# Performance work log

Hardware: AMD Instinct MI355X
Metric: run time of the kernel (lower is better)

The kernel has to match this reference:

```python
import jax, jax.numpy as jnp
import numpy as np

NUM_HEADS = 8
CODEBOOK_SIZE = 1024
HEAD_DIM = 128
BATCH = 32768


def setup_inputs() -> dict:
    key = jax.random.key(0)
    k_z, k_cb = jax.random.split(key)
    z = jax.random.normal(k_z, (BATCH, NUM_HEADS * HEAD_DIM), dtype=jnp.float32)
    codebooks = jax.random.normal(k_cb, (NUM_HEADS, CODEBOOK_SIZE, HEAD_DIM), dtype=jnp.float32)
    return {"z": z, "codebooks": codebooks}


def reference(z, codebooks):
    # z: [B, H*D]; codebooks: [H, K, D]
    H, K, D = codebooks.shape
    B = z.shape[0]
    zh = z.reshape(B, H, D)
    # Squared euclidean distances ||z - c||^2 = ||z||^2 - 2 z.c + ||c||^2.
    # torch.cdist(p=2) applies sqrt, but sqrt is monotone so argmin is identical.
    z_sq = jnp.sum(zh * zh, axis=-1)                       # [B, H]
    c_sq = jnp.sum(codebooks * codebooks, axis=-1)         # [H, K]
    cross = jnp.einsum('bhd,hkd->bhk', zh, codebooks)      # [B, H, K]
    d2 = z_sq[:, :, None] - 2.0 * cross + c_sq[None, :, :]  # [B, H, K]
    idx = jnp.argmin(d2, axis=-1)                          # [B, H] int
    # Gather nearest codes per head: codebooks[h, idx[b,h]] -> [B, H, D]
    zq = codebooks[jnp.arange(H)[None, :], idx]
    # Straight-through estimator: forward = codes, backward = identity on z.
    zq = zh + jax.lax.stop_gradient(zq - zh)
    return zq.reshape(B, H * D), idx
```

## Files before the change

kernel.cpp:

```cpp
#include <hip/hip_runtime.h>

namespace {
constexpr int kNH = 8;
constexpr int kK  = 1024;
constexpr int kD  = 128;
constexpr int kB  = 32768;

constexpr int BM  = 128;
constexpr int kMarginQ = 4;
constexpr float kMarginF32 = 0.0625f;

constexpr size_t kOffCsq  = 4096;
constexpr size_t kOffCbF  = 65536;
constexpr size_t kOffPart = 65536 + 4194304;
constexpr size_t kOffWl6  = 65536 + 8388608;
constexpr size_t kOffWl5  = 65536 + 4194304;
}

typedef short           bf16x8 __attribute__((ext_vector_type(8)));
typedef unsigned short  us16x8 __attribute__((ext_vector_type(8)));
typedef float           f32x16 __attribute__((ext_vector_type(16)));

__device__ __forceinline__ unsigned short f2bf_rne(float f) {
    unsigned int x = __float_as_uint(f);
    unsigned int r = (x + 0x7fffu + ((x >> 16) & 1u)) >> 16;
    return (unsigned short)r;
}
__device__ __forceinline__ float bf2f(unsigned short u) {
    return __uint_as_float(((unsigned int)u) << 16);
}
__device__ __forceinline__ int med3_i32(int a, int b, int c) {
    int d;
    asm("v_med3_i32 %0, %1, %2, %3" : "=v"(d) : "v"(a), "v"(b), "v"(c));
    return d;
}

__global__ void pq_prep(const float* __restrict__ cb,
                        unsigned short* __restrict__ cbf,
                        float* __restrict__ csq)
{
    int code = blockIdx.x;
    int t = threadIdx.x;
    int h = code >> 10, k = code & 1023;
    int kt = k >> 6, cv = (k >> 5) & 1, l31 = k & 31;
    int kc = t >> 4, hh = (t >> 3) & 1, j = t & 7;
    float v = cb[(size_t)code * kD + t];
    float vs = v * -2048.0f;
    unsigned short hb = f2bf_rne(vs);
    unsigned short lb = f2bf_rne(vs - bf2f(hb));
    size_t base = ((((size_t)h * 16 + kt) * 8 + kc) * 2 + cv) * 2048;
    size_t off  = base + (hh * 32 + l31) * 16 + j * 2;
    *(unsigned short*)((char*)cbf + off)        = hb;
    *(unsigned short*)((char*)cbf + off + 1024) = lb;
    __shared__ double red[128];
    red[t] = (double)v * (double)v;
    __syncthreads();
    for (int s = 64; s > 0; s >>= 1) {
        if (t < s) red[t] += red[t + s];
        __syncthreads();
    }
    if (t == 0) csq[code] = (float)(red[0] * 1024.0);
}

__global__ __launch_bounds__(512)
void pq_coarse_mfma7(const float* __restrict__ z,
                     const unsigned short* __restrict__ cbf,
                     const float* __restrict__ csq1024,
                     int2* __restrict__ part)
{
    __shared__ unsigned short zbuf[2][2][32 * kD];
    __shared__ int2  P[2][8][32];
    __shared__ float csel_s[8][2][2][16];

    const int t    = threadIdx.x;
    const int lane = t & 63;
    const int w    = t >> 6;
    const int l31  = lane & 31, h32 = lane >> 5;
    const int h    = blockIdx.y;
    const int half = blockIdx.z;
    const int rb0  = blockIdx.x * 1024;

    {
        int ww = t >> 6, hb2 = (t >> 5) & 1, idx = t & 31;
        int cv = idx >> 4, r = idx & 15;
        int cr = (r & 3) + ((r >> 2) << 3);
        csel_s[ww][hb2][cv][r] =
            csq1024[h * kK + half * 512 + ww * 64 + hb2 * 4 + cv * 32 + cr];
    }

    const int cgb = half * 512 + w * 64 + h32 * 4;
    int addv[2][16];
    #pragma unroll
    for (int cv = 0; cv < 2; ++cv)
        #pragma unroll
        for (int r = 0; r < 16; ++r)
            addv[cv][r] = cgb + cv * 32 + (r & 3) + ((r >> 2) << 3);

    bf16x8 Ah[8][2], Al[8][2];
    {
        const char* base = (const char*)cbf
            + (((size_t)h * 16 + half * 8 + w) * 16) * 2048 + lane * 16;
        #pragma unroll
        for (int kc = 0; kc < 8; ++kc)
            #pragma unroll
            for (int cv = 0; cv < 2; ++cv) {
                const char* p = base + (size_t)(kc * 2 + cv) * 2048;
                Ah[kc][cv] = *(const bf16x8*)p;
                Al[kc][cv] = *(const bf16x8*)(p + 1024);
            }
    }

    float4 zA, zB;
    auto issueZ = [&](int tile) {
        const float* zp = z + (size_t)(rb0 + tile * 32 + (t >> 4)) * (kNH * kD)
                            + h * kD + (t & 15) * 8;
        zA = *(const float4*)zp;
        zB = *(const float4*)(zp + 4);
    };
    auto commitZ = [&](int buf) {
        unsigned u0 = __float_as_uint(zA.x) + 0x8000u;
        unsigned u1 = __float_as_uint(zA.y) + 0x8000u;
        unsigned u2 = __float_as_uint(zA.z) + 0x8000u;
        unsigned u3 = __float_as_uint(zA.w) + 0x8000u;
        unsigned u4 = __float_as_uint(zB.x) + 0x8000u;
        unsigned u5 = __float_as_uint(zB.y) + 0x8000u;
        unsigned u6 = __float_as_uint(zB.z) + 0x8000u;
        unsigned u7 = __float_as_uint(zB.w) + 0x8000u;
        unsigned h01 = __builtin_amdgcn_perm(u1, u0, 0x07060302u);
        unsigned h23 = __builtin_amdgcn_perm(u3, u2, 0x07060302u);
        unsigned h45 = __builtin_amdgcn_perm(u5, u4, 0x07060302u);
        unsigned h67 = __builtin_amdgcn_perm(u7, u6, 0x07060302u);
        float r0 = zA.x - __uint_as_float(u0 & 0xffff0000u);
        float r1 = zA.y - __uint_as_float(u1 & 0xffff0000u);
        float r2 = zA.z - __uint_as_float(u2 & 0xffff0000u);
        float r3 = zA.w - __uint_as_float(u3 & 0xffff0000u);
        float r4 = zB.x - __uint_as_float(u4 & 0xffff0000u);
        float r5 = zB.y - __uint_as_float(u5 & 0xffff0000u);
        float r6 = zB.z - __uint_as_float(u6 & 0xffff0000u);
        float r7 = zB.w - __uint_as_float(u7 & 0xffff0000u);
        unsigned l01 = __builtin_amdgcn_perm(__float_as_uint(r1) + 0x8000u,
                                             __float_as_uint(r0) + 0x8000u, 0x07060302u);
        unsigned l23 = __builtin_amdgcn_perm(__float_as_uint(r3) + 0x8000u,
                                             __float_as_uint(r2) + 0x8000u, 0x07060302u);
        unsigned l45 = __builtin_amdgcn_perm(__float_as_uint(r5) + 0x8000u,
                                             __float_as_uint(r4) + 0x8000u, 0x07060302u);
        unsigned l67 = __builtin_amdgcn_perm(__float_as_uint(r7) + 0x8000u,
                                             __float_as_uint(r6) + 0x8000u, 0x07060302u);
        int rr = t >> 4, seg = t & 15;
        int off = rr * 256 + ((seg * 16) ^ ((rr & 15) << 4));
        uint4 hv = {h01, h23, h45, h67};
        uint4 lv = {l01, l23, l45, l67};
        *(uint4*)((char*)&zbuf[buf][0][0] + off) = hv;
        *(uint4*)((char*)&zbuf[buf][1][0] + off) = lv;
    };
    auto mergeP = [&](int pb, int tile) {
        int2 m = P[pb][0][t];
        int m1 = m.x, m2 = m.y;
        #pragma unroll
        for (int ww = 1; ww < 8; ++ww) {
            int2 p = P[pb][ww][t];
            int mx = max(m1, p.x);
            m1 = min(m1, p.x);
            m2 = min(min(m2, p.y), mx);
        }
        int gid = (rb0 + tile * 32 + t) * kNH + h;
        part[(size_t)gid * 2 + half] = make_int2(m1, m2);
    };

    issueZ(0);
    commitZ(0);
    __syncthreads();

    int cur = 0;
    for (int tile = 0; tile < 32; ++tile) {
        if (tile + 1 < 32) issueZ(tile + 1);
        if (tile > 0 && t < 32) mergeP(cur ^ 1, tile - 1);

        f32x16 acc0, acc1;
        __builtin_memcpy(&acc0, &csel_s[w][h32][0][0], 64);
        __builtin_memcpy(&acc1, &csel_s[w][h32][1][0], 64);

        const char* zh0 = (const char*)&zbuf[cur][0][0];
        const char* zl0 = (const char*)&zbuf[cur][1][0];
        const int boff = l31 * 256;
        const int swz  = (l31 & 15) << 4;
        #pragma unroll
        for (int kc = 0; kc < 8; ++kc) {
            int col = (kc * 32 + h32 * 16) ^ swz;
            bf16x8 Bh = *(const bf16x8*)(zh0 + boff + col);
            bf16x8 Bl = *(const bf16x8*)(zl0 + boff + col);
            __builtin_amdgcn_s_setprio(1);
            acc0 = __builtin_amdgcn_mfma_f32_32x32x16_bf16(Ah[kc][0], Bh, acc0, 0, 0, 0);
            acc1 = __builtin_amdgcn_mfma_f32_32x32x16_bf16(Ah[kc][1], Bh, acc1, 0, 0, 0);
            acc0 = __builtin_amdgcn_mfma_f32_32x32x16_bf16(Al[kc][0], Bh, acc0, 0, 0, 0);
            acc1 = __builtin_amdgcn_mfma_f32_32x32x16_bf16(Al[kc][1], Bh, acc1, 0, 0, 0);
            acc0 = __builtin_amdgcn_mfma_f32_32x32x16_bf16(Ah[kc][0], Bl, acc0, 0, 0, 0);
            acc1 = __builtin_amdgcn_mfma_f32_32x32x16_bf16(Ah[kc][1], Bl, acc1, 0, 0, 0);
            __builtin_amdgcn_s_setprio(0);
        }
        int b1 = 0x7fffffff, b2 = 0x7fffffff;
        #pragma unroll
        for (int r = 0; r < 16; ++r) {
            {
                int key = (((int)acc0[r]) << 10) + addv[0][r];
                b2 = med3_i32(key, b1, b2);
                b1 = min(b1, key);
            }
            {
                int key = (((int)acc1[r]) << 10) + addv[1][r];
                b2 = med3_i32(key, b1, b2);
                b1 = min(b1, key);
            }
        }
        int o1 = __shfl_xor(b1, 32), o2 = __shfl_xor(b2, 32);
        int mx2 = max(b1, o1);
        int v1 = min(b1, o1);
        int v2 = min(min(b2, o2), mx2);
        if (h32 == 0) P[cur][w][l31] = make_int2(v1, v2);

        if (tile + 1 < 32) commitZ(cur ^ 1);
        __syncthreads();
        cur ^= 1;
    }
    if (t < 32) mergeP(cur ^ 1, 31);
}

__global__ __launch_bounds__(256)
void pq_merge(const int2* __restrict__ part, const float* __restrict__ cb,
              float* __restrict__ out_zq, float* __restrict__ out_idx,
              unsigned int* wl_count, unsigned int* wl, unsigned int wl_cap)
{
    __shared__ int idx_s[128];
    const int t = threadIdx.x;
    const int g0 = blockIdx.x * 128;
    if (t < 128) {
        int gid = g0 + t;
        int2 p0 = part[(size_t)gid * 2];
        int2 p1 = part[(size_t)gid * 2 + 1];
        int mx = max(p0.x, p1.x);
        int v1 = min(p0.x, p1.x);
        int v2 = min(min(p0.y, p1.y), mx);
        int idx = v1 & 1023;
        idx_s[t] = idx;
        out_idx[gid] = (float)idx;
        if (wl_cap > 0u && ((v2 >> 10) - (v1 >> 10)) <= kMarginQ) {
            unsigned int pos = atomicAdd(wl_count, 1u);
            if (pos < wl_cap) wl[pos] = (unsigned int)gid;
        }
    }
    __syncthreads();
    #pragma unroll
    for (int it = 0; it < 16; ++it) {
        int c = it * 256 + t;
        int row = c >> 5, c4 = c & 31;
        int gid = g0 + row;
        int b = gid >> 3, hh = gid & 7;
        *(float4*)(out_zq + (size_t)b * (kNH * kD) + hh * kD + c4 * 4) =
            *(const float4*)(cb + ((size_t)hh * kK + idx_s[row]) * kD + c4 * 4);
    }
}

__global__ __launch_bounds__(256, 2)
void pq_coarse_mfma3(const float* __restrict__ z, const float* __restrict__ cb,
                     const unsigned short* __restrict__ cbf,
                     const float* __restrict__ csq1024,
                     float* __restrict__ out_zq, float* __restrict__ out_idx,
                     unsigned int* wl_count, unsigned int* wl, unsigned int wl_cap)
{
    __shared__ float csq_s[kK];
    __shared__ int   idx_s[BM];

    const int t    = threadIdx.x;
    const int h    = blockIdx.y;
    const int b0   = blockIdx.x * BM;
    const int lane = t & 63;
    const int w    = t >> 6;
    const int l31  = lane & 31, h32 = lane >> 5;

    *(float4*)&csq_s[t * 4] = *(const float4*)(csq1024 + h * kK + t * 4);

    bf16x8 Ah[8], Al[8];
    {
        const float* zr = z + (size_t)(b0 + w * 32 + l31) * (kNH * kD) + h * kD + h32 * 8;
        #pragma unroll
        for (int kc = 0; kc < 8; ++kc) {
            float4 a = *(const float4*)(zr + kc * 16);
            float4 b = *(const float4*)(zr + kc * 16 + 4);
            float f[8] = {a.x, a.y, a.z, a.w, b.x, b.y, b.z, b.w};
            bf16x8 hv, lv;
            #pragma unroll
            for (int j = 0; j < 8; ++j) {
                unsigned short hb = f2bf_rne(f[j]);
                hv[j] = (short)hb;
                lv[j] = (short)f2bf_rne(f[j] - bf2f(hb));
            }
            Ah[kc] = hv;
            Al[kc] = lv;
        }
    }
    __syncthreads();

    int b1[16], b2[16];
    #pragma unroll
    for (int r = 0; r < 16; ++r) { b1[r] = 0x7fffffff; b2[r] = 0x7fffffff; }

    const char* bbase = (const char*)cbf + (size_t)h * 524288 + lane * 16;
#define LDSLOT(kt_, kc_, s_)                                                  \
    {                                                                         \
        const char* p_ = bbase + (size_t)(((kt_) * 8 + (kc_)) * 2) * 2048;    \
        Bh0[s_] = *(const bf16x8*)(p_);                                       \
        Bl0[s_] = *(const bf16x8*)(p_ + 1024);                                \
        Bh1[s_] = *(const bf16x8*)(p_ + 2048);                                \
        Bl1[s_] = *(const bf16x8*)(p_ + 3072);                                \
    }

    bf16x8 Bh0[4], Bl0[4], Bh1[4], Bl1[4];
    LDSLOT(0, 0, 0);
    LDSLOT(0, 1, 1);

    for (int kt = 0; kt < 16; ++kt) {
        f32x16 acc0 = (f32x16)0.0f, acc1 = (f32x16)0.0f;
        const int ktn = (kt + 1 < 16) ? kt + 1 : kt;
        #pragma unroll
        for (int kc = 0; kc < 8; ++kc) {
            const int s  = kc & 3;
            const int s2 = (kc + 2) & 3;
            if (kc < 6) { LDSLOT(kt, kc + 2, s2); } else { LDSLOT(ktn, kc - 6, s2); }
            __builtin_amdgcn_s_setprio(1);
            acc0 = __builtin_amdgcn_mfma_f32_32x32x16_bf16(Ah[kc], Bh0[s], acc0, 0, 0, 0);
            acc1 = __builtin_amdgcn_mfma_f32_32x32x16_bf16(Ah[kc], Bh1[s], acc1, 0, 0, 0);
            acc0 = __builtin_amdgcn_mfma_f32_32x32x16_bf16(Al[kc], Bh0[s], acc0, 0, 0, 0);
            acc1 = __builtin_amdgcn_mfma_f32_32x32x16_bf16(Al[kc], Bh1[s], acc1, 0, 0, 0);
            acc0 = __builtin_amdgcn_mfma_f32_32x32x16_bf16(Ah[kc], Bl0[s], acc0, 0, 0, 0);
            acc1 = __builtin_amdgcn_mfma_f32_32x32x16_bf16(Ah[kc], Bl1[s], acc1, 0, 0, 0);
            __builtin_amdgcn_s_setprio(0);
        }
        const float cs0 = csq_s[kt * 64 + l31];
        const float cs1 = csq_s[kt * 64 + 32 + l31];
        const int   kg0 = kt * 64 + l31, kg1 = kg0 + 32;
        #pragma unroll
        for (int r = 0; r < 16; ++r) {
            {
                float kf = acc0[r] + cs0;
                int key = ((int)kf << 10) + kg0;
                int mx = max(b1[r], key); b1[r] = min(b1[r], key); b2[r] = min(b2[r], mx);
            }
            {
                float kf = acc1[r] + cs1;
                int key = ((int)kf << 10) + kg1;
                int mx = max(b1[r], key); b1[r] = min(b1[r], key); b2[r] = min(b2[r], mx);
            }
        }
    }
#undef LDSLOT

    #pragma unroll
    for (int r = 0; r < 16; ++r) {
        int v1 = b1[r], v2 = b2[r];
        #pragma unroll
        for (int m = 1; m < 32; m <<= 1) {
            int o1 = __shfl_xor(v1, m);
            int o2 = __shfl_xor(v2, m);
            int mx = max(v1, o1);
            v1 = min(v1, o1);
            v2 = min(min(v2, o2), mx);
        }
        if (l31 == 0) {
            int row = w * 32 + (r & 3) + ((r >> 2) << 3) + h32 * 4;
            int idx = v1 & 1023;
            idx_s[row] = idx;
            int gid = (b0 + row) * kNH + h;
            out_idx[gid] = (float)idx;
            if (wl_cap > 0u && ((v2 >> 10) - (v1 >> 10)) <= kMarginQ) {
                unsigned int pos = atomicAdd(wl_count, 1u);
                if (pos < wl_cap) wl[pos] = (unsigned int)gid;
            }
        }
    }
    __syncthreads();
    {
        const float* cbh_row = cb + (size_t)h * kK * kD;
        #pragma unroll
        for (int it = 0; it < 16; ++it) {
            int c = it * 256 + t;
            int row = c >> 5, col4 = c & 31;
            *(float4*)(out_zq + (size_t)(b0 + row) * (kNH * kD) + h * kD + col4 * 4) =
                *(const float4*)(cbh_row + (size_t)idx_s[row] * kD + col4 * 4);
        }
    }
}

__global__ __launch_bounds__(256, 2)
void pq_coarse_f32(const float* __restrict__ z, const float* __restrict__ cb,
                   float* __restrict__ out_zq, float* __restrict__ out_idx,
                   unsigned int* wl_count, unsigned int* wl, unsigned int wl_cap)
{
    constexpr int KT = 64, PAD = 68, BMF = 64;
    __shared__ float zT[kD][PAD];
    __shared__ float cT[kD][PAD];
    __shared__ float csq_s[KT];
    __shared__ int   bidx_s[BMF];

    const int t  = threadIdx.x;
    const int h  = blockIdx.y;
    const int b0 = blockIdx.x * BMF;
    const int tx = t & 15, ty = t >> 4;
    const int r8 = t & 7,  d4 = t >> 3;

    {
        const float* zp = z + (size_t)(b0 + r8) * (kNH * kD) + h * kD + 4 * d4;
        #pragma unroll
        for (int it = 0; it < BMF / 8; ++it) {
            float4 v = *(const float4*)(zp + (size_t)(8 * it) * (kNH * kD));
            int r = r8 + 8 * it;
            zT[4 * d4 + 0][r] = v.x; zT[4 * d4 + 1][r] = v.y;
            zT[4 * d4 + 2][r] = v.z; zT[4 * d4 + 3][r] = v.w;
        }
    }
    float best1[4], best2[4]; int ibest[4];
    #pragma unroll
    for (int i = 0; i < 4; ++i) { best1[i] = 3.4e38f; best2[i] = 3.4e38f; ibest[i] = 0; }

    for (int kt = 0; kt < kK / KT; ++kt) {
        __syncthreads();
        {
            const float* cp = cb + ((size_t)h * kK + kt * KT + r8) * kD + 4 * d4;
            #pragma unroll
            for (int it = 0; it < KT / 8; ++it) {
                float4 v = *(const float4*)(cp + (size_t)(8 * it) * kD);
                int r = r8 + 8 * it;
                cT[4 * d4 + 0][r] = v.x; cT[4 * d4 + 1][r] = v.y;
                cT[4 * d4 + 2][r] = v.z; cT[4 * d4 + 3][r] = v.w;
            }
        }
        if (t < KT) csq_s[t] = 0.0f;
        __syncthreads();
        {
            int kk = t & 63, part = t >> 6;
            float s = 0.f;
            #pragma unroll
            for (int i = 0; i < 32; ++i) { float v = cT[32 * part + i][kk]; s = fmaf(v, v, s); }
            atomicAdd(&csq_s[kk], s);
        }
        __syncthreads();
        float accA[4][4] = {{0}}, accB[4][4] = {{0}};
        #pragma unroll 2
        for (int d = 0; d < kD; d += 2) {
            float4 za = *(const float4*)&zT[d][4 * ty];
            float4 ca = *(const float4*)&cT[d][4 * tx];
            float4 zb = *(const float4*)&zT[d + 1][4 * ty];
            float4 cv = *(const float4*)&cT[d + 1][4 * tx];
            float zav[4] = {za.x, za.y, za.z, za.w}, cav[4] = {ca.x, ca.y, ca.z, ca.w};
            float zbv[4] = {zb.x, zb.y, zb.z, zb.w}, cbv[4] = {cv.x, cv.y, cv.z, cv.w};
            #pragma unroll
            for (int i = 0; i < 4; ++i)
                #pragma unroll
                for (int j = 0; j < 4; ++j) {
                    accA[i][j] = fmaf(zav[i], cav[j], accA[i][j]);
                    accB[i][j] = fmaf(zbv[i], cbv[j], accB[i][j]);
                }
        }
        #pragma unroll
        for (int j = 0; j < 4; ++j) {
            int kk = 4 * tx + j;
            float cs = csq_s[kk];
            int kg = kt * KT + kk;
            #pragma unroll
            for (int i = 0; i < 4; ++i) {
                float s = fmaf(-2.0f, accA[i][j] + accB[i][j], cs);
                if (s < best1[i]) { best2[i] = best1[i]; best1[i] = s; ibest[i] = kg; }
                else if (s < best2[i]) { best2[i] = s; }
            }
        }
    }
    __syncthreads();
    float* redv1 = &zT[0][0];
    float* redv2 = redv1 + BMF * 16;
    int*   redi  = (int*)(redv2 + BMF * 16);
    #pragma unroll
    for (int i = 0; i < 4; ++i) {
        int r = 4 * ty + i;
        redv1[r * 16 + tx] = best1[i]; redv2[r * 16 + tx] = best2[i]; redi[r * 16 + tx] = ibest[i];
    }
    __syncthreads();
    if (t < BMF) {
        int r = t;
        float vb1_ = redv1[r * 16], vb2_ = redv2[r * 16];
        int i1 = redi[r * 16];
        #pragma unroll
        for (int x = 1; x < 16; ++x) {
            float nb1 = redv1[r * 16 + x], nb2 = redv2[r * 16 + x];
            int ni1 = redi[r * 16 + x];
            if (nb1 < vb1_ || (nb1 == vb1_ && ni1 < i1)) { vb2_ = fminf(vb1_, nb2); vb1_ = nb1; i1 = ni1; }
            else vb2_ = fminf(vb2_, nb1);
        }
        bidx_s[r] = i1;
        int gid = (b0 + r) * kNH + h;
        out_idx[gid] = (float)i1;
        if (wl_cap > 0u && (vb2_ - vb1_) <= kMarginF32) {
            unsigned int pos = atomicAdd(wl_count, 1u);
            if (pos < wl_cap) wl[pos] = (unsigned int)gid;
        }
    }
    __syncthreads();
    {
        int r = t >> 2, q = t & 3;
        const float* src = cb + ((size_t)h * kK + bidx_s[r]) * kD;
        float* dst = out_zq + (size_t)(b0 + r) * (kNH * kD) + h * kD;
        #pragma unroll
        for (int m = 0; m < 8; ++m) {
            int jj = 4 * m + q;
            *(float4*)(dst + 4 * jj) = *(const float4*)(src + 4 * jj);
        }
    }
}

__global__ __launch_bounds__(256)
void pq_exact(const float* __restrict__ z, const float* __restrict__ cb,
              float* __restrict__ out_zq, float* __restrict__ out_idx,
              const unsigned int* wl_count, const unsigned int* wl,
              unsigned int wl_cap)
{
    if (wl_cap == 0u) return;
    __shared__ float  zs[kD];
    __shared__ double rv[256];
    __shared__ int    ri[256];
    unsigned int n = *wl_count;
    if (n > wl_cap) n = wl_cap;
    const int t = threadIdx.x;
    for (unsigned int e = blockIdx.x; e < n; e += gridDim.x) {
        unsigned int id = wl[e];
        int b = (int)(id / kNH), h = (int)(id % kNH);
        if (t < kD) zs[t] = z[(size_t)b * (kNH * kD) + h * kD + t];
        __syncthreads();
        double bv = 1e300; int bi = 0;
        #pragma unroll
        for (int kk = 0; kk < 4; ++kk) {
            int k = t * 4 + kk;
            const float* c = cb + ((size_t)h * kK + k) * kD;
            double s = 0.0;
            for (int d = 0; d < kD; ++d) {
                double diff = (double)zs[d] - (double)c[d];
                s = fma(diff, diff, s);
            }
            if (s < bv) { bv = s; bi = k; }
        }
        rv[t] = bv; ri[t] = bi;
        __syncthreads();
        for (int s2 = 128; s2 > 0; s2 >>= 1) {
            if (t < s2) {
                if (rv[t + s2] < rv[t] || (rv[t + s2] == rv[t] && ri[t + s2] < ri[t])) {
                    rv[t] = rv[t + s2]; ri[t] = ri[t + s2];
                }
            }
            __syncthreads();
        }
        int kbest = ri[0];
        if (t == 0) out_idx[id] = (float)kbest;
        if (t < kD)
            out_zq[(size_t)b * (kNH * kD) + h * kD + t] =
                cb[((size_t)h * kK + kbest) * kD + t];
        __syncthreads();
    }
}

extern "C" void kernel_launch(void* const* d_in, const int* in_sizes, int n_in,
                              void* d_out, int out_size, void* d_ws, size_t ws_size,
                              hipStream_t stream)
{
    const float* z  = (const float*)d_in[0];
    const float* cb = (const float*)d_in[1];
    float* out_zq  = (float*)d_out;
    float* out_idx = out_zq + (size_t)kB * kNH * kD;
    char* ws = (char*)d_ws;

    if (ws_size >= kOffWl6 + 65536) {
        unsigned int* wl_count = (unsigned int*)ws;
        unsigned int* wl = (unsigned int*)(ws + kOffWl6);
        size_t c = (ws_size - kOffWl6) / 4;
        unsigned int cap = (unsigned int)(c > 262144 ? 262144 : c);
        float* csq = (float*)(ws + kOffCsq);
        unsigned short* cbf = (unsigned short*)(ws + kOffCbF);
        int2* part = (int2*)(ws + kOffPart);

        hipMemsetAsync(d_ws, 0, 4, stream);
        pq_prep<<<kNH * kK, kD, 0, stream>>>(cb, cbf, csq);
        dim3 grid(32, kNH, 2);
        pq_coarse_mfma7<<<grid, 512, 0, stream>>>(z, cbf, csq, part);
        pq_merge<<<kB * kNH / 128, 256, 0, stream>>>(part, cb, out_zq, out_idx,
                                                     wl_count, wl, cap);
        pq_exact<<<256, 256, 0, stream>>>(z, cb, out_zq, out_idx, wl_count, wl, cap);
    } else if (ws_size >= kOffWl5 + 4096) {
        unsigned int* wl_count = (unsigned int*)ws;
        unsigned int* wl = (unsigned int*)(ws + kOffWl5);
        size_t c = (ws_size - kOffWl5) / 4;
        unsigned int cap = (unsigned int)(c > 262144 ? 262144 : c);
        float* csq = (float*)(ws + kOffCsq);
        unsigned short* cbf = (unsigned short*)(ws + kOffCbF);

        hipMemsetAsync(d_ws, 0, 4, stream);
        pq_prep<<<kNH * kK, kD, 0, stream>>>(cb, cbf, csq);
        dim3 grid(kB / BM, kNH);
        pq_coarse_mfma3<<<grid, 256, 0, stream>>>(z, cb, cbf, csq,
                                                  out_zq, out_idx, wl_count, wl, cap);
        pq_exact<<<256, 256, 0, stream>>>(z, cb, out_zq, out_idx, wl_count, wl, cap);
    } else {
        unsigned int* wl_count = (unsigned int*)ws;
        unsigned int* wl = wl_count + 1;
        unsigned int cap = 0;
        if (ws_size >= 64) {
            size_t c = ws_size / 4 - 1;
            cap = (unsigned int)(c > 262144 ? 262144 : c);
            hipMemsetAsync(d_ws, 0, 4, stream);
        }
        dim3 grid(kB / 64, kNH);
        pq_coarse_f32<<<grid, 256, 0, stream>>>(z, cb, out_zq, out_idx, wl_count, wl, cap);
        pq_exact<<<256, 256, 0, stream>>>(z, cb, out_zq, out_idx, wl_count, wl, cap);
    }
}
```

Before: 228.7 us.

## Split codebook into quarters per block and merge partial top-2 with atomicMin

The coarse MFMA kernel now gives each block a quarter of the codebook (256 codes) instead of half, so each wave keeps one 32-code accumulator and half the A-fragments in registers. The grid doubles in z to 4, which raises block count and should lower register pressure and improve occupancy. Partial top-2 keys are merged in global memory with two atomicMin operations on a buffer pre-filled by a memset, which replaces the two-slot partial array and simplifies the merge kernel. The cost is re-reading and re-converting z four times per head instead of twice, plus atomic traffic and an extra memset. The second-best update from the atomics is approximate under races, which could shift which rows land on the exact-recheck worklist.

```diff
diff --git a/kernel.cpp b/kernel.cpp
--- a/kernel.cpp
+++ b/kernel.cpp
@@ -13,12 +13,11 @@
 constexpr size_t kOffCsq  = 4096;
 constexpr size_t kOffCbF  = 65536;
 constexpr size_t kOffPart = 65536 + 4194304;
-constexpr size_t kOffWl6  = 65536 + 8388608;
+constexpr size_t kOffWl9  = 65536 + 4194304 + 2097152;
 constexpr size_t kOffWl5  = 65536 + 4194304;
 }
 
 typedef short           bf16x8 __attribute__((ext_vector_type(8)));
-typedef unsigned short  us16x8 __attribute__((ext_vector_type(8)));
 typedef float           f32x16 __attribute__((ext_vector_type(16)));
 
 __device__ __forceinline__ unsigned short f2bf_rne(float f) {
@@ -63,51 +62,46 @@
 }
 
 __global__ __launch_bounds__(512)
-void pq_coarse_mfma7(const float* __restrict__ z,
+void pq_coarse_mfma9(const float* __restrict__ z,
                      const unsigned short* __restrict__ cbf,
                      const float* __restrict__ csq1024,
                      int2* __restrict__ part)
 {
     __shared__ unsigned short zbuf[2][2][32 * kD];
     __shared__ int2  P[2][8][32];
-    __shared__ float csel_s[8][2][2][16];
+    __shared__ float csel_s[8][2][16];
 
     const int t    = threadIdx.x;
     const int lane = t & 63;
     const int w    = t >> 6;
     const int l31  = lane & 31, h32 = lane >> 5;
     const int h    = blockIdx.y;
-    const int half = blockIdx.z;
+    const int quar = blockIdx.z;
     const int rb0  = blockIdx.x * 1024;
 
-    {
-        int ww = t >> 6, hb2 = (t >> 5) & 1, idx = t & 31;
-        int cv = idx >> 4, r = idx & 15;
-        int cr = (r & 3) + ((r >> 2) << 3);
-        csel_s[ww][hb2][cv][r] =
-            csq1024[h * kK + half * 512 + ww * 64 + hb2 * 4 + cv * 32 + cr];
-    }
-
-    const int cgb = half * 512 + w * 64 + h32 * 4;
-    int addv[2][16];
+    if (t < 256) {
+        int ww = t >> 5, hb = (t >> 4) & 1, r = t & 15;
+        int cr = (r & 3) + ((r >> 2) << 3) + hb * 4;
+        csel_s[ww][hb][r] = csq1024[h * kK + quar * 256 + ww * 32 + cr];
+    }
+
+    int addv[16];
     #pragma unroll
-    for (int cv = 0; cv < 2; ++cv)
-        #pragma unroll
-        for (int r = 0; r < 16; ++r)
-            addv[cv][r] = cgb + cv * 32 + (r & 3) + ((r >> 2) << 3);
-
-    bf16x8 Ah[8][2], Al[8][2];
+    for (int r = 0; r < 16; ++r)
+        addv[r] = quar * 256 + w * 32 + (r & 3) + ((r >> 2) << 3) + h32 * 4;
+
+    const int cb32 = quar * 8 + w;
+    bf16x8 Ah[8], Al[8];
     {
         const char* base = (const char*)cbf
-            + (((size_t)h * 16 + half * 8 + w) * 16) * 2048 + lane * 16;
-        #pragma unroll
-        for (int kc = 0; kc < 8; ++kc)
-            #pragma unroll
-            for (int cv = 0; cv < 2; ++cv) {
-                const char* p = base + (size_t)(kc * 2 + cv) * 2048;
-                Ah[kc][cv] = *(const bf16x8*)p;
-                Al[kc][cv] = *(const bf16x8*)(p + 1024);
-            }
+            + ((((size_t)h * 16 + (cb32 >> 1)) * 8) * 2 + (cb32 & 1)) * 2048
+            + lane * 16;
+        #pragma unroll
+        for (int kc = 0; kc < 8; ++kc) {
+            const char* p = base + (size_t)(kc * 2) * 2048;
+            Ah[kc] = *(const bf16x8*)p;
+            Al[kc] = *(const bf16x8*)(p + 1024);
+        }
     }
 
     float4 zA, zB;
@@ -164,7 +158,8 @@
             m2 = min(min(m2, p.y), mx);
         }
         int gid = (rb0 + tile * 32 + t) * kNH + h;
-        part[(size_t)gid * 2 + half] = make_int2(m1, m2);
+        int old1 = atomicMin(&part[gid].x, m1);
+        atomicMin(&part[gid].y, min(max(old1, m1), m2));
     };
 
     issueZ(0);
@@ -176,41 +171,30 @@
         if (tile + 1 < 32) issueZ(tile + 1);
         if (tile > 0 && t < 32) mergeP(cur ^ 1, tile - 1);
 
-        f32x16 acc0, acc1;
-        __builtin_memcpy(&acc0, &csel_s[w][h32][0][0], 64);
-        __builtin_memcpy(&acc1, &csel_s[w][h32][1][0], 64);
+        f32x16 acc;
+        __builtin_memcpy(&acc, &csel_s[w][h32][0], 64);
 
         const char* zh0 = (const char*)&zbuf[cur][0][0];
         const char* zl0 = (const char*)&zbuf[cur][1][0];
         const int boff = l31 * 256;
         const int swz  = (l31 & 15) << 4;
+        __builtin_amdgcn_s_setprio(1);
         #pragma unroll
         for (int kc = 0; kc < 8; ++kc) {
             int col = (kc * 32 + h32 * 16) ^ swz;
             bf16x8 Bh = *(const bf16x8*)(zh0 + boff + col);
             bf16x8 Bl = *(const bf16x8*)(zl0 + boff + col);
-            __builtin_amdgcn_s_setprio(1);
-            acc0 = __builtin_amdgcn_mfma_f32_32x32x16_bf16(Ah[kc][0], Bh, acc0, 0, 0, 0);
-            acc1 = __builtin_amdgcn_mfma_f32_32x32x16_bf16(Ah[kc][1], Bh, acc1, 0, 0, 0);
-            acc0 = __builtin_amdgcn_mfma_f32_32x32x16_bf16(Al[kc][0], Bh, acc0, 0, 0, 0);
-            acc1 = __builtin_amdgcn_mfma_f32_32x32x16_bf16(Al[kc][1], Bh, acc1, 0, 0, 0);
-            acc0 = __builtin_amdgcn_mfma_f32_32x32x16_bf16(Ah[kc][0], Bl, acc0, 0, 0, 0);
-            acc1 = __builtin_amdgcn_mfma_f32_32x32x16_bf16(Ah[kc][1], Bl, acc1, 0, 0, 0);
-            __builtin_amdgcn_s_setprio(0);
-        }
+            acc = __builtin_amdgcn_mfma_f32_32x32x16_bf16(Ah[kc], Bh, acc, 0, 0, 0);
+            acc = __builtin_amdgcn_mfma_f32_32x32x16_bf16(Al[kc], Bh, acc, 0, 0, 0);
+            acc = __builtin_amdgcn_mfma_f32_32x32x16_bf16(Ah[kc], Bl, acc, 0, 0, 0);
+        }
+        __builtin_amdgcn_s_setprio(0);
         int b1 = 0x7fffffff, b2 = 0x7fffffff;
         #pragma unroll
         for (int r = 0; r < 16; ++r) {
-            {
-                int key = (((int)acc0[r]) << 10) + addv[0][r];
-                b2 = med3_i32(key, b1, b2);
-                b1 = min(b1, key);
-            }
-            {
-                int key = (((int)acc1[r]) << 10) + addv[1][r];
-                b2 = med3_i32(key, b1, b2);
-                b1 = min(b1, key);
-            }
+            int key = (((int)acc[r]) << 10) + addv[r];
+            b2 = med3_i32(key, b1, b2);
+            b1 = min(b1, key);
         }
         int o1 = __shfl_xor(b1, 32), o2 = __shfl_xor(b2, 32);
         int mx2 = max(b1, o1);
@@ -235,15 +219,11 @@
     const int g0 = blockIdx.x * 128;
     if (t < 128) {
         int gid = g0 + t;
-        int2 p0 = part[(size_t)gid * 2];
-        int2 p1 = part[(size_t)gid * 2 + 1];
-        int mx = max(p0.x, p1.x);
-        int v1 = min(p0.x, p1.x);
-        int v2 = min(min(p0.y, p1.y), mx);
-        int idx = v1 & 1023;
+        int2 p = part[gid];
+        int idx = p.x & 1023;
         idx_s[t] = idx;
         out_idx[gid] = (float)idx;
-        if (wl_cap > 0u && ((v2 >> 10) - (v1 >> 10)) <= kMarginQ) {
+        if (wl_cap > 0u && ((p.y >> 10) - (p.x >> 10)) <= kMarginQ) {
             unsigned int pos = atomicAdd(wl_count, 1u);
             if (pos < wl_cap) wl[pos] = (unsigned int)gid;
         }
@@ -574,19 +554,20 @@
     float* out_idx = out_zq + (size_t)kB * kNH * kD;
     char* ws = (char*)d_ws;
 
-    if (ws_size >= kOffWl6 + 65536) {
+    if (ws_size >= kOffWl9 + 65536) {
         unsigned int* wl_count = (unsigned int*)ws;
-        unsigned int* wl = (unsigned int*)(ws + kOffWl6);
-        size_t c = (ws_size - kOffWl6) / 4;
+        unsigned int* wl = (unsigned int*)(ws + kOffWl9);
+        size_t c = (ws_size - kOffWl9) / 4;
         unsigned int cap = (unsigned int)(c > 262144 ? 262144 : c);
         float* csq = (float*)(ws + kOffCsq);
         unsigned short* cbf = (unsigned short*)(ws + kOffCbF);
         int2* part = (int2*)(ws + kOffPart);
 
         hipMemsetAsync(d_ws, 0, 4, stream);
+        hipMemsetAsync(part, 0x7f, (size_t)kB * kNH * 8, stream);
         pq_prep<<<kNH * kK, kD, 0, stream>>>(cb, cbf, csq);
-        dim3 grid(32, kNH, 2);
-        pq_coarse_mfma7<<<grid, 512, 0, stream>>>(z, cbf, csq, part);
+        dim3 grid(32, kNH, 4);
+        pq_coarse_mfma9<<<grid, 512, 0, stream>>>(z, cbf, csq, part);
         pq_merge<<<kB * kNH / 128, 256, 0, stream>>>(part, cb, out_zq, out_idx,
                                                      wl_count, wl, cap);
         pq_exact<<<256, 256, 0, stream>>>(z, cb, out_zq, out_idx, wl_count, wl, cap);
```

Result: slower. 265.1 us (+15.9%).
